# Kernel tuning notes

Hardware: AMD Instinct MI355X
Metric: run time of the kernel (lower is better)

## Reference

```python
import jax, jax.numpy as jnp
import numpy as np

B, S, E, H, V, NCAT = 64, 100, 256, 256, 100000, 18


def _lstm_layer(x, Wih, Whh, bih, bhh):
    # x: [S, B, in], Wih: [4H, in], Whh: [4H, H]; PyTorch gate order i,f,g,o
    h0 = jnp.zeros((x.shape[1], Whh.shape[1]), x.dtype)

    def step(carry, xt):
        h, c = carry
        g = xt @ Wih.T + h @ Whh.T + bih + bhh
        i, f, gg, o = jnp.split(g, 4, axis=-1)
        c = jax.nn.sigmoid(f) * c + jax.nn.sigmoid(i) * jnp.tanh(gg)
        h = jax.nn.sigmoid(o) * jnp.tanh(c)
        return (h, c), h

    _, ys = jax.lax.scan(step, (h0, h0), x)
    return ys


def _lstm2_last(x, p):
    # x: [B, S, E]; p: 8-tuple of layer0/layer1 weights. Returns h at last step of top layer.
    x = jnp.swapaxes(x, 0, 1)  # [S, B, E]
    y = _lstm_layer(x, p[0], p[1], p[2], p[3])
    y = _lstm_layer(y, p[4], p[5], p[6], p[7])
    return y[-1]  # [B, H]


def setup_inputs() -> dict:
    key = jax.random.key(0)
    ks = jax.random.split(key, 24)
    sc = 0.05
    def n(k, shape):
        return jax.random.normal(k, shape, dtype=jnp.float32) * sc
    inp = {
        'input_vu': jax.random.randint(ks[0], (B, S), 0, V),
        'input_vo': jax.random.randint(ks[1], (B, S), 0, V),
        'label_ro': jax.random.uniform(ks[2], (B, NCAT), dtype=jnp.float32),
        'video_embeddings': n(ks[4], (V, E)),
    }
    u = jax.random.uniform(ks[3], (B, NCAT), dtype=jnp.float32) + 1e-3
    inp['label_ru'] = u / u.sum(-1, keepdims=True)  # valid prob dist (KL target)
    # lstm_vu params (2 layers)
    inp['vu_Wih0'] = n(ks[5], (4 * H, E)); inp['vu_Whh0'] = n(ks[6], (4 * H, H))
    inp['vu_bih0'] = n(ks[7], (4 * H,));  inp['vu_bhh0'] = n(ks[8], (4 * H,))
    inp['vu_Wih1'] = n(ks[9], (4 * H, H)); inp['vu_Whh1'] = n(ks[10], (4 * H, H))
    inp['vu_bih1'] = n(ks[11], (4 * H,)); inp['vu_bhh1'] = n(ks[12], (4 * H,))
    # lstm_vo params
    inp['vo_Wih0'] = n(ks[13], (4 * H, E)); inp['vo_Whh0'] = n(ks[14], (4 * H, H))
    inp['vo_bih0'] = n(ks[15], (4 * H,)); inp['vo_bhh0'] = n(ks[16], (4 * H,))
    inp['vo_Wih1'] = n(ks[17], (4 * H, H)); inp['vo_Whh1'] = n(ks[18], (4 * H, H))
    inp['vo_bih1'] = n(ks[19], (4 * H,)); inp['vo_bhh1'] = n(ks[20], (4 * H,))
    # linears
    inp['ro_W'] = n(ks[21], (H, NCAT)); inp['ro_b'] = jnp.zeros((H,), jnp.float32)
    inp['ru_W'] = n(ks[22], (NCAT, 3 * H)); inp['ru_b'] = jnp.zeros((NCAT,), jnp.float32)
    return inp


def reference(input_vu, input_vo, label_ro, label_ru, video_embeddings,
              vu_Wih0, vu_Whh0, vu_bih0, vu_bhh0, vu_Wih1, vu_Whh1, vu_bih1, vu_bhh1,
              vo_Wih0, vo_Whh0, vo_bih0, vo_bhh0, vo_Wih1, vo_Whh1, vo_bih1, vo_bhh1,
              ro_W, ro_b, ru_W, ru_b):
    emb_vu = video_embeddings[input_vu]  # [B,S,E] gather
    emb_vo = video_embeddings[input_vo]
    h_vu = _lstm2_last(emb_vu, (vu_Wih0, vu_Whh0, vu_bih0, vu_bhh0,
                                vu_Wih1, vu_Whh1, vu_bih1, vu_bhh1))
    h_vo = _lstm2_last(emb_vo, (vo_Wih0, vo_Whh0, vo_bih0, vo_bhh0,
                                vo_Wih1, vo_Whh1, vo_bih1, vo_bhh1))
    enc_ro = jax.nn.relu(label_ro @ ro_W.T + ro_b)
    dec = jnp.concatenate([h_vu, h_vo, enc_ro], axis=-1) @ ru_W.T + ru_b  # [B,18]
    logp = jax.nn.log_softmax(dec, axis=-1)
    neg_logits = -(label_ru * logp).sum(-1)  # [B]
    pred = jax.nn.softmax(dec, axis=-1)
    # fused batched KL: mean_i sum_j p_ij * log2(p_ij / q_ij)
    avg_kl = (label_ru * jnp.log2(label_ru / pred)).sum(-1).mean()
    return (neg_logits, avg_kl)
```

## Files before the change

kernel.cpp:

```cpp
#include <hip/hip_runtime.h>
#include <math.h>

#define S_LEN 100
#define NCAT  18
#define HS    516
#define WSTR  520
#define G_OFF 524288

typedef __attribute__((ext_vector_type(8)))  short  short8;
typedef __attribute__((ext_vector_type(16))) float  floatx16;

#define AT_LOADU(p)   __hip_atomic_load((p), __ATOMIC_RELAXED, __HIP_MEMORY_SCOPE_AGENT)
#define AT_STORE(p,v) __hip_atomic_store((p),(v), __ATOMIC_RELAXED, __HIP_MEMORY_SCOPE_AGENT)


struct Params {
  const int* ivu; const int* ivo;
  const float* lro; const float* lru;
  const float* VE;
  const float* W[4][2];
  const float* b0[4]; const float* b1[4];
  const float* roW; const float* rob;
  const float* ruW; const float* rub;
  float* ws; float* out;
};

__device__ __forceinline__ unsigned short f2bf(float f) {
  unsigned u = __builtin_bit_cast(unsigned, f);
  u += 0x7FFFu + ((u >> 16) & 1u);
  return (unsigned short)(u >> 16);
}
__device__ __forceinline__ float bf2f(unsigned short h) {
  unsigned u = ((unsigned)h) << 16;
  return __builtin_bit_cast(float, u);
}
__device__ __forceinline__ unsigned long long packbf4(float4 v) {
  return (unsigned long long)f2bf(v.x)
       | ((unsigned long long)f2bf(v.y) << 16)
       | ((unsigned long long)f2bf(v.z) << 32)
       | ((unsigned long long)f2bf(v.w) << 48);
}
__device__ __forceinline__ float sigm(float x) {
  return __builtin_amdgcn_rcpf(1.f + __expf(-x));
}
__device__ __forceinline__ float tanh_f(float x) {
  return 1.f - 2.f * __builtin_amdgcn_rcpf(1.f + __expf(2.f * x));
}

__global__ __launch_bounds__(256) void gate0_k(Params P) {
  const int tid = threadIdx.x;
  char* wsb = (char*)P.ws;
  if (blockIdx.x == 3200) {
    ((unsigned*)(wsb + 262144))[tid] = 0u;
    if (tid == 0) P.out[64] = 0.f;
    return;
  }
  const int blk = blockIdx.x;
  const int inst = blk / 1600;
  const int rem = blk - inst * 1600;
  const int t = rem >> 4, wg = rem & 15;
  const int lane = tid & 63, wave = tid >> 6;
  const int jt = wave >> 1, bt = wave & 1, half = lane >> 5;
  const int trow = lane & 31;
  const int R = (trow & 3) * 256 + wg * 16 + jt * 8 + (trow >> 2);
  const int b = bt * 32 + trow;
  const int* __restrict__ idxp = inst ? P.ivo : P.ivu;
  const float* __restrict__ wih = P.W[inst][0] + (size_t)R * 256;
  const float* __restrict__ vr = P.VE + (size_t)idxp[b * S_LEN + t] * 256;

  floatx16 acc;
  #pragma unroll
  for (int r = 0; r < 16; ++r) {
    const int Rr = (r & 3) * 256 + wg * 16 + jt * 8 + 2 * (r >> 2) + half;
    acc[r] = P.b0[inst][Rr] + P.b1[inst][Rr];
  }
  #pragma unroll
  for (int s = 0; s < 16; ++s) {
    float4 a0 = *(const float4*)(wih + s * 16 + half * 8);
    float4 a1 = *(const float4*)(wih + s * 16 + half * 8 + 4);
    float4 e0 = *(const float4*)(vr + s * 16 + half * 8);
    float4 e1 = *(const float4*)(vr + s * 16 + half * 8 + 4);
    union { unsigned long long q[2]; short8 v; } ua, ub;
    ua.q[0] = packbf4(a0); ua.q[1] = packbf4(a1);
    ub.q[0] = packbf4(e0); ub.q[1] = packbf4(e1);
    acc = __builtin_amdgcn_mfma_f32_32x32x16_bf16(ua.v, ub.v, acc, 0, 0, 0);
  }
  float* gd = (float*)((char*)P.ws + G_OFF) + (size_t)blk * 4096 + tid * 16;
  *(floatx16*)gd = acc;
}

__global__ __launch_bounds__(256, 1) void lstm_all(Params P) {
  __shared__ short          Wlds[64 * WSTR];
  __shared__ unsigned short hstage[64 * HS];

  const int tid  = threadIdx.x;
  const int lane = tid & 63;
  const int wave = tid >> 6;
  const int rbk  = blockIdx.x;
  const int xcd  = rbk & 7, grpi = rbk >> 3;
  const int lstm = xcd >> 2;
  const int idx32 = grpi * 4 + (xcd & 3);
  const int layer = idx32 >> 4;
  const int wg    = idx32 & 15;
  const int inst  = layer * 2 + lstm;
  const int gb    = idx32;

  char* wsb = (char*)P.ws;
  unsigned* arr = (unsigned*)(wsb + 262144) + lstm * 128;

  const int jt = wave >> 1, bt = wave & 1;
  const int half = lane >> 5;
  const int trow = lane & 31;
  const int bl   = bt * 32 + trow;

  {
    const int jrow = tid >> 2;
    const int q    = tid & 3;
    const int tr   = jrow & 31, jts = jrow >> 5;
    const int R    = (tr & 3) * 256 + wg * 16 + jts * 8 + (tr >> 2);
    const float* wih = P.W[inst][0] + (size_t)R * 256;
    const float* whh = P.W[inst][1] + (size_t)R * 256;
    short* dst = &Wlds[jrow * WSTR];
    if (layer || q < 2) {
      #pragma unroll
      for (int k = q * 128; k < q * 128 + 128; k += 8) {
        const float* src = layer ? ((k < 256) ? (wih + k) : (whh + (k - 256)))
                                 : (whh + k);
        float4 v0 = *(const float4*)src;
        float4 v1 = *(const float4*)(src + 4);
        *(unsigned long long*)(dst + k)     = packbf4(v0);
        *(unsigned long long*)(dst + k + 4) = packbf4(v1);
      }
    }
  }
  float bias16[16];
  if (layer) {
    #pragma unroll
    for (int r = 0; r < 16; ++r) {
      const int Rr = (r & 3) * 256 + wg * 16 + jt * 8 + 2 * (r >> 2) + half;
      bias16[r] = P.b0[inst][Rr] + P.b1[inst][Rr];
    }
  }

  #pragma unroll
  for (int j = 0; j < 2; ++j) {
    const int gi = gb * 512 + tid * 2 + j;
    const int r = gi >> 12, off = gi & 4095;
    char* base = wsb + ((r < 2) ? (size_t)(lstm * 2 + r) * 32768
                                : 131072 + (size_t)(lstm * 2 + r - 2) * 32768);
    AT_STORE((unsigned long long*)base + off, 0ull);
  }
  __syncthreads();
  if (tid == 0) AT_STORE(arr + gb * 4, 1u);

  const int arow_off = (jt * 32 + trow) * WSTR + half * 8;
  const int brow_off = bl * HS + half * 8;
  const float* __restrict__ gregion = (const float*)(wsb + G_OFF);

  floatx16 gcur;
  if (layer == 0)
    gcur = *(const floatx16*)(gregion
             + (size_t)((lstm * 100) * 16 + wg) * 4096 + tid * 16);
  float c[4] = {0.f, 0.f, 0.f, 0.f};

  for (int t = 0; t <= S_LEN; ++t) {
    if (wave == 0) {
      const unsigned want = (unsigned)(t + 1);
      const unsigned* slot = arr + trow * 4;
      while (!__all(AT_LOADU(slot) >= want)) { }
    }
    __syncthreads();

    const bool active = (layer == 0) ? (t < S_LEN) : (t >= 1);
    if (active) {
      const int cur = t & 1, prv = (t + 1) & 1;

      if (layer == 0) {
        const unsigned long long* s64 =
            (const unsigned long long*)(wsb + (size_t)(lstm * 2 + prv) * 32768);
        unsigned long long v[16];
        #pragma unroll
        for (int j = 0; j < 16; ++j) v[j] = AT_LOADU(s64 + tid + j * 256);
        #pragma unroll
        for (int j = 0; j < 16; ++j) {
          const int i = tid + j * 256, bb = i >> 6, kq = i & 63;
          *(unsigned long long*)&hstage[bb * HS + kq * 4] = v[j];
        }
      } else {
        const unsigned long long* lo =
            (const unsigned long long*)(wsb + (size_t)(lstm * 2 + prv) * 32768);
        const unsigned long long* hi =
            (const unsigned long long*)(wsb + 131072 + (size_t)(lstm * 2 + cur) * 32768);
        unsigned long long v[32];
        #pragma unroll
        for (int j = 0; j < 16; ++j) v[j]      = AT_LOADU(lo + tid + j * 256);
        #pragma unroll
        for (int j = 0; j < 16; ++j) v[16 + j] = AT_LOADU(hi + tid + j * 256);
        #pragma unroll
        for (int j = 0; j < 16; ++j) {
          const int i = tid + j * 256, bb = i >> 6, kq = i & 63;
          *(unsigned long long*)&hstage[bb * HS + kq * 4] = v[j];
        }
        #pragma unroll
        for (int j = 0; j < 16; ++j) {
          const int i = tid + j * 256, bb = i >> 6, kq = i & 63;
          *(unsigned long long*)&hstage[bb * HS + 256 + kq * 4] = v[16 + j];
        }
      }
      __syncthreads();

      floatx16 acc, acc2;
      if (layer == 0) {
        acc = gcur;
        #pragma unroll
        for (int r = 0; r < 16; ++r) acc2[r] = 0.f;
        #pragma unroll
        for (int s = 0; s < 16; s += 2) {
          short8 a0 = *(const short8*)&Wlds[arow_off + s * 16];
          short8 b0 = *(const short8*)&hstage[brow_off + s * 16];
          short8 a1 = *(const short8*)&Wlds[arow_off + (s + 1) * 16];
          short8 b1 = *(const short8*)&hstage[brow_off + (s + 1) * 16];
          acc  = __builtin_amdgcn_mfma_f32_32x32x16_bf16(a0, b0, acc,  0, 0, 0);
          acc2 = __builtin_amdgcn_mfma_f32_32x32x16_bf16(a1, b1, acc2, 0, 0, 0);
        }
      } else {
        #pragma unroll
        for (int r = 0; r < 16; ++r) { acc[r] = bias16[r]; acc2[r] = 0.f; }
        #pragma unroll
        for (int s = 0; s < 32; s += 2) {
          short8 a0 = *(const short8*)&Wlds[arow_off + s * 16];
          short8 b0 = *(const short8*)&hstage[brow_off + s * 16];
          short8 a1 = *(const short8*)&Wlds[arow_off + (s + 1) * 16];
          short8 b1 = *(const short8*)&hstage[brow_off + (s + 1) * 16];
          acc  = __builtin_amdgcn_mfma_f32_32x32x16_bf16(a0, b0, acc,  0, 0, 0);
          acc2 = __builtin_amdgcn_mfma_f32_32x32x16_bf16(a1, b1, acc2, 0, 0, 0);
        }
      }
      #pragma unroll
      for (int r = 0; r < 16; ++r) acc[r] += acc2[r];

      unsigned long long own = 0ull;
      #pragma unroll
      for (int q = 0; q < 4; ++q) {
        const float ig = sigm(acc[4 * q + 0]);
        const float fg = sigm(acc[4 * q + 1]);
        const float gg = tanh_f(acc[4 * q + 2]);
        const float og = sigm(acc[4 * q + 3]);
        const float cc = fg * c[q] + ig * gg;
        c[q] = cc;
        own |= ((unsigned long long)f2bf(og * tanh_f(cc))) << (16 * q);
      }
      {
        const unsigned long long oth =
            (unsigned long long)__shfl_xor((long long)own, 32, 64);
        const unsigned long long A = half ? oth : own;
        const unsigned long long B = half ? own : oth;
        const unsigned a32 = half ? (unsigned)(A >> 32) : (unsigned)A;
        const unsigned b32 = half ? (unsigned)(B >> 32) : (unsigned)B;
        const unsigned long long pack =
              (unsigned long long)(a32 & 0xFFFFu)
            | ((unsigned long long)(b32 & 0xFFFFu) << 16)
            | ((unsigned long long)(a32 >> 16) << 32)
            | ((unsigned long long)(b32 >> 16) << 48);
        unsigned long long* hout = (layer == 0)
            ? (unsigned long long*)(wsb + (size_t)(lstm * 2 + cur) * 32768)
            : (unsigned long long*)(wsb + 131072 + (size_t)(lstm * 2 + prv) * 32768);
        AT_STORE(hout + bl * 64 + wg * 4 + jt * 2 + half, pack);
      }
    }
    if (t < S_LEN) {
      __syncthreads();
      if (tid == 0) AT_STORE(arr + gb * 4, (unsigned)(t + 2));
    }
    if (layer == 0 && t + 1 < S_LEN)
      gcur = *(const floatx16*)(gregion
               + (size_t)((lstm * 100 + t + 1) * 16 + wg) * 4096 + tid * 16);
  }
}

__global__ __launch_bounds__(64) void head_kernel(Params P) {
  __shared__ float enc[256];
  __shared__ float dec[NCAT];
  const int b = blockIdx.x, t = threadIdx.x;
  char* wsb = (char*)P.ws;
  const unsigned short* hvu = (const unsigned short*)(wsb + 131072 + 1 * 32768) + b * 256;
  const unsigned short* hvo = (const unsigned short*)(wsb + 131072 + 3 * 32768) + b * 256;

  for (int m = t; m < 256; m += 64) {
    float s = P.rob[m];
    for (int j = 0; j < NCAT; ++j) s = fmaf(P.lro[b * NCAT + j], P.roW[m * NCAT + j], s);
    enc[m] = fmaxf(s, 0.f);
  }
  __syncthreads();
  for (int n = 0; n < NCAT; ++n) {
    const float* __restrict__ wr = P.ruW + n * 768;
    float s = 0.f;
    for (int k = t; k < 256; k += 64) {
      s = fmaf(bf2f(hvu[k]), wr[k], s);
      s = fmaf(bf2f(hvo[k]), wr[256 + k], s);
      s = fmaf(enc[k],       wr[512 + k], s);
    }
    for (int off = 32; off; off >>= 1) s += __shfl_down(s, off, 64);
    if (t == 0) dec[n] = s + P.rub[n];
  }
  __syncthreads();
  if (t == 0) {
    float M = dec[0];
    for (int j = 1; j < NCAT; ++j) M = fmaxf(M, dec[j]);
    float Ssum = 0.f;
    for (int j = 0; j < NCAT; ++j) Ssum += expf(dec[j] - M);
    const float lse = M + logf(Ssum);
    float neg = 0.f, kl = 0.f;
    for (int j = 0; j < NCAT; ++j) {
      const float lp = dec[j] - lse;
      const float q  = P.lru[b * NCAT + j];
      neg -= q * lp;
      kl  += q * (logf(q) - lp);
    }
    P.out[b] = neg;
    atomicAdd(&P.out[64], kl * 1.4426950408889634f * (1.f / 64.f));
  }
}

extern "C" void kernel_launch(void* const* d_in, const int* in_sizes, int n_in,
                              void* d_out, int out_size, void* d_ws, size_t ws_size,
                              hipStream_t stream) {
  Params P;
  P.ivu = (const int*)d_in[0];
  P.ivo = (const int*)d_in[1];
  P.lro = (const float*)d_in[2];
  if (in_sizes[3] >= in_sizes[4]) { P.VE = (const float*)d_in[3]; P.lru = (const float*)d_in[4]; }
  else                            { P.VE = (const float*)d_in[4]; P.lru = (const float*)d_in[3]; }
  P.W[0][0] = (const float*)d_in[5];  P.W[0][1] = (const float*)d_in[6];
  P.b0[0]   = (const float*)d_in[7];  P.b1[0]   = (const float*)d_in[8];
  P.W[2][0] = (const float*)d_in[9];  P.W[2][1] = (const float*)d_in[10];
  P.b0[2]   = (const float*)d_in[11]; P.b1[2]   = (const float*)d_in[12];
  P.W[1][0] = (const float*)d_in[13]; P.W[1][1] = (const float*)d_in[14];
  P.b0[1]   = (const float*)d_in[15]; P.b1[1]   = (const float*)d_in[16];
  P.W[3][0] = (const float*)d_in[17]; P.W[3][1] = (const float*)d_in[18];
  P.b0[3]   = (const float*)d_in[19]; P.b1[3]   = (const float*)d_in[20];
  P.roW = (const float*)d_in[21]; P.rob = (const float*)d_in[22];
  P.ruW = (const float*)d_in[23]; P.rub = (const float*)d_in[24];
  P.ws  = (float*)d_ws;
  P.out = (float*)d_out;

  gate0_k<<<dim3(3201), dim3(256), 0, stream>>>(P);
  lstm_all<<<dim3(64), dim3(256), 0, stream>>>(P);
  head_kernel<<<dim3(64), dim3(64), 0, stream>>>(P);
}
```

Before: 728.7 us.

## Fuse gate precompute into persistent LSTM kernel with per-tile ready flags

Gate-projection work is folded into the LSTM kernel as extra blocks that store tiles and set per-tile flags. The recurrent blocks spin-wait on those flags before loading each timestep's gate tile, so the recurrence can start before all precompute finishes. Flag and stat zeroing move to memsets. The static LDS of the fused kernel limits how many gate blocks fit per CU, and relaxed flag ordering may be fragile.

```diff
diff --git a/kernel.cpp b/kernel.cpp
--- a/kernel.cpp
+++ b/kernel.cpp
@@ -5,7 +5,9 @@
 #define NCAT  18
 #define HS    516
 #define WSTR  520
-#define G_OFF 524288
+#define FLG_OFF  262144
+#define GFLG_OFF 263168
+#define G_OFF    524288
 
 typedef __attribute__((ext_vector_type(8)))  short  short8;
 typedef __attribute__((ext_vector_type(16))) float  floatx16;
@@ -47,19 +49,27 @@
   return 1.f - 2.f * __builtin_amdgcn_rcpf(1.f + __expf(2.f * x));
 }
 
-__global__ __launch_bounds__(256) void gate0_k(Params P) {
-  const int tid = threadIdx.x;
+__device__ __forceinline__ floatx16 load_gtile(const char* wsb, int idx, int tid) {
+  const unsigned long long* gp =
+      (const unsigned long long*)(wsb + G_OFF + (size_t)idx * 16384) + tid * 8;
+  floatx16 g;
+  #pragma unroll
+  for (int j = 0; j < 8; ++j) {
+    union { unsigned long long u; float f[2]; } cv;
+    cv.u = AT_LOADU(gp + j);
+    g[2 * j] = cv.f[0]; g[2 * j + 1] = cv.f[1];
+  }
+  return g;
+}
+
+__device__ __forceinline__ void gate0_body(const Params& P, int idx) {
   char* wsb = (char*)P.ws;
-  if (blockIdx.x == 3200) {
-    ((unsigned*)(wsb + 262144))[tid] = 0u;
-    if (tid == 0) P.out[64] = 0.f;
-    return;
-  }
-  const int blk = blockIdx.x;
-  const int inst = blk / 1600;
-  const int rem = blk - inst * 1600;
-  const int t = rem >> 4, wg = rem & 15;
-  const int lane = tid & 63, wave = tid >> 6;
+  const int t = idx >> 5;
+  const int r = idx & 31;
+  const int inst = r >> 4, wg = r & 15;
+  const int blk = (inst * 100 + t) * 16 + wg;
+
+  const int tid = threadIdx.x, lane = tid & 63, wave = tid >> 6;
   const int jt = wave >> 1, bt = wave & 1, half = lane >> 5;
   const int trow = lane & 31;
   const int R = (trow & 3) * 256 + wg * 16 + jt * 8 + (trow >> 2);
@@ -70,9 +80,9 @@
 
   floatx16 acc;
   #pragma unroll
-  for (int r = 0; r < 16; ++r) {
-    const int Rr = (r & 3) * 256 + wg * 16 + jt * 8 + 2 * (r >> 2) + half;
-    acc[r] = P.b0[inst][Rr] + P.b1[inst][Rr];
+  for (int rr = 0; rr < 16; ++rr) {
+    const int Rr = (rr & 3) * 256 + wg * 16 + jt * 8 + 2 * (rr >> 2) + half;
+    acc[rr] = P.b0[inst][Rr] + P.b1[inst][Rr];
   }
   #pragma unroll
   for (int s = 0; s < 16; ++s) {
@@ -85,13 +95,23 @@
     ub.q[0] = packbf4(e0); ub.q[1] = packbf4(e1);
     acc = __builtin_amdgcn_mfma_f32_32x32x16_bf16(ua.v, ub.v, acc, 0, 0, 0);
   }
-  float* gd = (float*)((char*)P.ws + G_OFF) + (size_t)blk * 4096 + tid * 16;
-  *(floatx16*)gd = acc;
+  unsigned long long* gd =
+      (unsigned long long*)(wsb + G_OFF + (size_t)blk * 16384) + tid * 8;
+  #pragma unroll
+  for (int j = 0; j < 8; ++j) {
+    union { float f[2]; unsigned long long u; } cv;
+    cv.f[0] = acc[2 * j]; cv.f[1] = acc[2 * j + 1];
+    AT_STORE(gd + j, cv.u);
+  }
+  __syncthreads();
+  if (tid == 0) AT_STORE((unsigned*)(wsb + GFLG_OFF) + blk, 1u);
 }
 
 __global__ __launch_bounds__(256, 1) void lstm_all(Params P) {
   __shared__ short          Wlds[64 * WSTR];
   __shared__ unsigned short hstage[64 * HS];
+
+  if (blockIdx.x >= 64) { gate0_body(P, (int)blockIdx.x - 64); return; }
 
   const int tid  = threadIdx.x;
   const int lane = tid & 63;
@@ -106,7 +126,7 @@
   const int gb    = idx32;
 
   char* wsb = (char*)P.ws;
-  unsigned* arr = (unsigned*)(wsb + 262144) + lstm * 128;
+  unsigned* arr = (unsigned*)(wsb + FLG_OFF) + lstm * 128;
 
   const int jt = wave >> 1, bt = wave & 1;
   const int half = lane >> 5;
@@ -155,12 +175,14 @@
 
   const int arow_off = (jt * 32 + trow) * WSTR + half * 8;
   const int brow_off = bl * HS + half * 8;
-  const float* __restrict__ gregion = (const float*)(wsb + G_OFF);
+  const unsigned* __restrict__ gflags = (const unsigned*)(wsb + GFLG_OFF);
 
   floatx16 gcur;
-  if (layer == 0)
-    gcur = *(const floatx16*)(gregion
-             + (size_t)((lstm * 100) * 16 + wg) * 4096 + tid * 16);
+  if (layer == 0) {
+    const int gidx = (lstm * 100) * 16 + wg;
+    while (AT_LOADU(gflags + gidx) == 0) { }
+    gcur = load_gtile(wsb, gidx, tid);
+  }
   float c[4] = {0.f, 0.f, 0.f, 0.f};
 
   for (int t = 0; t <= S_LEN; ++t) {
@@ -272,9 +294,11 @@
       __syncthreads();
       if (tid == 0) AT_STORE(arr + gb * 4, (unsigned)(t + 2));
     }
-    if (layer == 0 && t + 1 < S_LEN)
-      gcur = *(const floatx16*)(gregion
-               + (size_t)((lstm * 100 + t + 1) * 16 + wg) * 4096 + tid * 16);
+    if (layer == 0 && t + 1 < S_LEN) {
+      const int gidx = (lstm * 100 + t + 1) * 16 + wg;
+      while (AT_LOADU(gflags + gidx) == 0) { }
+      gcur = load_gtile(wsb, gidx, tid);
+    }
   }
 }
 
@@ -344,7 +368,9 @@
   P.ws  = (float*)d_ws;
   P.out = (float*)d_out;
 
-  gate0_k<<<dim3(3201), dim3(256), 0, stream>>>(P);
-  lstm_all<<<dim3(64), dim3(256), 0, stream>>>(P);
+  hipMemsetAsync((char*)d_ws + FLG_OFF, 0, 16384, stream);
+  hipMemsetAsync((char*)d_out + 64 * sizeof(float), 0, sizeof(float), stream);
+
+  lstm_all<<<dim3(3264), dim3(256), 0, stream>>>(P);
   head_kernel<<<dim3(64), dim3(64), 0, stream>>>(P);
 }
```

New measurement: 635.8 us. -12.8%, faster.
